# Performance work log

Hardware: AMD Instinct MI355X
Metric: run time of the kernel (lower is better)

## Reference

```python
import jax, jax.numpy as jnp
import numpy as np

B, N, D, E, H = 4, 1024, 1024, 8, 4096


def setup_inputs() -> dict:
    key = jax.random.key(0)
    ks = jax.random.split(key, 8)
    x = jax.random.normal(ks[0], (B, N, D), dtype=jnp.float32)
    # gumbel noise, matching F.gumbel_softmax's -log(-log(U))
    u = jax.random.uniform(ks[1], (B * N, E), dtype=jnp.float32, minval=1e-9, maxval=1.0)
    gumbel = -jnp.log(-jnp.log(u))
    router_w = jax.random.normal(ks[2], (D, E), dtype=jnp.float32) * 0.02
    router_b = jnp.zeros((E,), dtype=jnp.float32)
    w1 = jax.random.normal(ks[3], (E, D, H), dtype=jnp.float32) * 0.02
    b1 = jnp.zeros((E, H), dtype=jnp.float32)
    w2 = jax.random.normal(ks[4], (E, H, D), dtype=jnp.float32) * 0.02
    b2 = jnp.zeros((E, D), dtype=jnp.float32)
    return {"x": x, "gumbel": gumbel, "router_w": router_w, "router_b": router_b,
            "w1": w1, "b1": b1, "w2": w2, "b2": b2}


def reference(x, gumbel, router_w, router_b, w1, b1, w2, b2):
    b, n, d = x.shape
    e = router_w.shape[1]
    xf = x.reshape(-1, d)                      # (T, D), T = B*N tokens
    logits = xf @ router_w + router_b          # (T, E)

    # hard gumbel-softmax with straight-through estimator (tau = 1.0)
    y_soft = jax.nn.softmax(logits + gumbel, axis=-1)
    hard = jax.nn.one_hot(jnp.argmax(y_soft, axis=-1), e, dtype=y_soft.dtype)
    weights = hard - jax.lax.stop_gradient(y_soft) + y_soft   # (T, E)

    # load-balancing aux loss
    probs = jax.nn.softmax(logits, axis=-1)
    count = jnp.maximum(jnp.float32(xf.shape[0]), 1.0)
    importance = probs.sum(axis=0) / count
    aux_loss = jnp.mean((importance - 1.0 / e) ** 2)

    # dense all-expert FFN: every expert processes every token
    hidden = jax.nn.gelu(jnp.einsum('td,edh->eth', xf, w1) + b1[:, None, :],
                         approximate=False)                    # (E, T, H)
    expert_out = jnp.einsum('eth,ehd->etd', hidden, w2) + b2[:, None, :]  # (E, T, D)

    # weighted combine (einsum 'ej,ejd->jd' in the original)
    out = jnp.einsum('te,etd->td', weights, expert_out)        # (T, D)
    return out.reshape(b, n, d), aux_loss
```

## Files before the change

kernel.cpp:

```cpp
#include <hip/hip_runtime.h>
#include <math.h>

#define D_DIM 1024
#define MAX_TILES 40

typedef __attribute__((ext_vector_type(4))) float f32x4;
typedef __attribute__((ext_vector_type(8))) short s16x8;

__device__ __forceinline__ unsigned short f2bf(float f){
  union { float f; unsigned u; } v; v.f = f;
  unsigned r = v.u + 0x7FFFu + ((v.u >> 16) & 1u);
  return (unsigned short)(r >> 16);
}

__device__ __forceinline__ void gld_lds16(const unsigned short* g, unsigned short* l){
  __builtin_amdgcn_global_load_lds(
      (const __attribute__((address_space(1))) unsigned int*)g,
      (__attribute__((address_space(3))) unsigned int*)l, 16, 0, 0);
}

__global__ __launch_bounds__(256) void router_kernel(
    const float* __restrict__ x, const float* __restrict__ gumbel,
    const float* __restrict__ rw, const float* __restrict__ rb,
    int* __restrict__ expert_id, float* __restrict__ wtok,
    double* __restrict__ prob_sums, int* __restrict__ counts)
{
  int wave = threadIdx.x >> 6, lane = threadIdx.x & 63;
  int t = blockIdx.x * 4 + wave;
  const float* xr = x + (size_t)t * D_DIM;
  double acc[8];
  #pragma unroll
  for (int e = 0; e < 8; e++) acc[e] = 0.0;
  #pragma unroll
  for (int i = 0; i < 16; i++){
    int d = i * 64 + lane;
    double xv = (double)xr[d];
    const float4* rwp = (const float4*)(rw + (size_t)d * 8);
    float4 r0 = rwp[0], r1 = rwp[1];
    acc[0] += xv * (double)r0.x; acc[1] += xv * (double)r0.y;
    acc[2] += xv * (double)r0.z; acc[3] += xv * (double)r0.w;
    acc[4] += xv * (double)r1.x; acc[5] += xv * (double)r1.y;
    acc[6] += xv * (double)r1.z; acc[7] += xv * (double)r1.w;
  }
  #pragma unroll
  for (int e = 0; e < 8; e++){
    #pragma unroll
    for (int off = 32; off; off >>= 1) acc[e] += __shfl_xor(acc[e], off);
  }
  double logit[8], z[8];
  #pragma unroll
  for (int e = 0; e < 8; e++){
    logit[e] = acc[e] + (double)rb[e];
    z[e] = logit[e] + (double)gumbel[(size_t)t * 8 + e];
  }
  int amax = 0;
  #pragma unroll
  for (int e = 1; e < 8; e++) if (z[e] > z[amax]) amax = e;
  float zm = (float)z[amax];
  float se = 0.f;
  #pragma unroll
  for (int e = 0; e < 8; e++) se += expf((float)z[e] - zm);
  float y = 1.f / se;
  float w = (1.0f - y) + y;
  double lm = logit[0];
  #pragma unroll
  for (int e = 1; e < 8; e++) lm = fmax(lm, logit[e]);
  float p[8]; float ps = 0.f;
  #pragma unroll
  for (int e = 0; e < 8; e++){ p[e] = expf((float)(logit[e] - lm)); ps += p[e]; }
  float inv = 1.f / ps;

  __shared__ float sprob[4][8];
  if (lane == 0){
    expert_id[t] = amax; wtok[t] = w;
    atomicAdd(&counts[amax], 1);
    #pragma unroll
    for (int e = 0; e < 8; e++) sprob[wave][e] = p[e] * inv;
  }
  __syncthreads();
  if (threadIdx.x < 8){
    double s = (double)sprob[0][threadIdx.x] + (double)sprob[1][threadIdx.x]
             + (double)sprob[2][threadIdx.x] + (double)sprob[3][threadIdx.x];
    atomicAdd(&prob_sums[threadIdx.x], s);
  }
}

__global__ void finalize_kernel(const double* __restrict__ prob_sums, const int* __restrict__ counts,
                                int* __restrict__ offsets, int* __restrict__ cursor,
                                int* __restrict__ tile_e, int* __restrict__ tile_start,
                                int* __restrict__ tile_rows, int* __restrict__ n_mtiles,
                                float* __restrict__ aux_out)
{
  if (threadIdx.x == 0){
    int off = 0, m = 0;
    for (int e = 0; e < 8; e++){
      offsets[e] = off; cursor[e] = off;
      int c = counts[e];
      for (int by = 0; by * 128 < c; by++){
        tile_e[m] = e;
        tile_start[m] = off + by * 128;
        int r = c - by * 128;
        tile_rows[m] = r < 128 ? r : 128;
        m++;
      }
      off += c;
    }
    n_mtiles[0] = m;
    double aux = 0.0;
    for (int e = 0; e < 8; e++){
      double d = prob_sums[e] / 4096.0 - 0.125;
      aux += d * d;
    }
    aux_out[0] = (float)(aux / 8.0);
  }
}

__global__ __launch_bounds__(256) void scatter_kernel(
    const float* __restrict__ x, const int* __restrict__ expert_id, const float* __restrict__ wtok,
    int* __restrict__ cursor, int* __restrict__ token_of, float* __restrict__ gw,
    unsigned short* __restrict__ Xg)
{
  int t = blockIdx.x;
  __shared__ int spos;
  if (threadIdx.x == 0){
    int e = expert_id[t];
    int p = atomicAdd(&cursor[e], 1);
    spos = p;
    token_of[p] = t; gw[p] = wtok[t];
  }
  __syncthreads();
  int pos = spos;
  float4 v = ((const float4*)(x + (size_t)t * D_DIM))[threadIdx.x];
  ushort4 o; o.x = f2bf(v.x); o.y = f2bf(v.y); o.z = f2bf(v.z); o.w = f2bf(v.w);
  ((ushort4*)(Xg + (size_t)pos * D_DIM))[threadIdx.x] = o;
}

__global__ __launch_bounds__(256) void transpose_w(
    const float* __restrict__ W, unsigned short* __restrict__ WT, int K, int N)
{
  int e = blockIdx.z;
  int k0 = blockIdx.x * 64;
  int n0 = blockIdx.y * 64;
  __shared__ float tile[64][65];
  const float* src = W + (size_t)e * K * N;
  int tid = threadIdx.x;
  int r = tid >> 4;
  int c4 = (tid & 15) * 4;
  #pragma unroll
  for (int j = 0; j < 4; j++){
    int k = r + j * 16;
    float4 v = *(const float4*)(src + (size_t)(k0 + k) * N + n0 + c4);
    tile[k][c4] = v.x; tile[k][c4 + 1] = v.y; tile[k][c4 + 2] = v.z; tile[k][c4 + 3] = v.w;
  }
  __syncthreads();
  unsigned short* dst = WT + (size_t)e * N * K;
  int n = tid >> 2;
  #pragma unroll
  for (int h = 0; h < 2; h++){
    int s = (tid & 3) + h * 4;
    unsigned short buf[8];
    #pragma unroll
    for (int j = 0; j < 8; j++) buf[j] = f2bf(tile[s * 8 + j][n]);
    *(s16x8*)(dst + (size_t)(n0 + n) * K + k0 + s * 8) = *(s16x8*)buf;
  }
}

template<int K, int N, int BN, int PASS2>
__global__ __launch_bounds__(256, 2) void ffn_gemm(
    const unsigned short* __restrict__ A,
    const unsigned short* __restrict__ BT,
    const float* __restrict__ bias,
    const int* __restrict__ tile_e, const int* __restrict__ tile_start,
    const int* __restrict__ tile_rows, const int* __restrict__ n_mtiles,
    const int* __restrict__ token_of, const float* __restrict__ gw,
    unsigned short* __restrict__ Hout,
    float* __restrict__ Fout)
{
  int mt = blockIdx.y;
  if (mt >= n_mtiles[0]) return;
  int e = tile_e[mt], tstart = tile_start[mt], trows = tile_rows[mt];
  int bx = blockIdx.x;
  int tid = threadIdx.x, lane = tid & 63;
  int wv = __builtin_amdgcn_readfirstlane(tid >> 6);
  int wm = wv & 1, wn = wv >> 1;
  constexpr int NI  = BN / 32;
  constexpr int NBW = BN / 32;
  constexpr int NK  = K / 64;

  __shared__ unsigned short sA[2][128 * 64];
  __shared__ unsigned short sB[2][BN * 64];

  int r8  = lane >> 3;
  int swz = ((lane & 7) ^ r8) * 8;

  const unsigned short* ap[4]; int al[4];
  #pragma unroll
  for (int j = 0; j < 4; j++){
    int c = wv * 4 + j;
    int row = c * 8 + r8;
    int rr = row < trows ? row : 0;
    ap[j] = A + (size_t)(tstart + rr) * K + swz;
    al[j] = c * 512;
  }
  const unsigned short* bp[NBW]; int bl[NBW];
  #pragma unroll
  for (int j = 0; j < NBW; j++){
    int c = wv * NBW + j;
    int n = bx * BN + c * 8 + r8;
    bp[j] = BT + ((size_t)e * N + n) * K + swz;
    bl[j] = c * 512;
  }

  f32x4 accv[4][NI];
  #pragma unroll
  for (int mi = 0; mi < 4; mi++)
    #pragma unroll
    for (int ni = 0; ni < NI; ni++) accv[mi][ni] = (f32x4){0.f, 0.f, 0.f, 0.f};

  #pragma unroll
  for (int j = 0; j < 4; j++){ gld_lds16(ap[j], &sA[0][al[j]]); ap[j] += 64; }
  #pragma unroll
  for (int j = 0; j < NBW; j++){ gld_lds16(bp[j], &sB[0][bl[j]]); bp[j] += 64; }
  __syncthreads();

  int col = lane & 15, quad = lane >> 4, rx = col & 7;
  for (int kt = 0; kt < NK; ++kt){
    int cur = kt & 1;
    if (kt + 1 < NK){
      #pragma unroll
      for (int j = 0; j < 4; j++){ gld_lds16(ap[j], &sA[cur ^ 1][al[j]]); ap[j] += 64; }
      #pragma unroll
      for (int j = 0; j < NBW; j++){ gld_lds16(bp[j], &sB[cur ^ 1][bl[j]]); bp[j] += 64; }
    }
    #pragma unroll
    for (int kh = 0; kh < 2; kh++){
      int ps = ((kh * 4 + quad) ^ rx) * 8;
      s16x8 af[4], bfr[NI];
      #pragma unroll
      for (int mi = 0; mi < 4; mi++)
        af[mi] = *(const s16x8*)&sA[cur][(wm * 64 + mi * 16 + col) * 64 + ps];
      #pragma unroll
      for (int ni = 0; ni < NI; ni++)
        bfr[ni] = *(const s16x8*)&sB[cur][(wn * (BN / 2) + ni * 16 + col) * 64 + ps];
      #pragma unroll
      for (int mi = 0; mi < 4; mi++)
        #pragma unroll
        for (int ni = 0; ni < NI; ni++)
          accv[mi][ni] = __builtin_amdgcn_mfma_f32_16x16x32_bf16(af[mi], bfr[ni], accv[mi][ni], 0, 0, 0);
    }
    __syncthreads();
  }

  float bv[NI];
  #pragma unroll
  for (int ni = 0; ni < NI; ni++)
    bv[ni] = bias[(size_t)e * N + bx * BN + wn * (BN / 2) + ni * 16 + col];

  if (PASS2 == 0){
    #pragma unroll
    for (int mi = 0; mi < 4; mi++){
      int rbase = wm * 64 + mi * 16 + quad * 4;
      #pragma unroll
      for (int r = 0; r < 4; r++){
        int row = rbase + r;
        if (row < trows){
          size_t orow = (size_t)(tstart + row) * N + bx * BN + wn * (BN / 2) + col;
          #pragma unroll
          for (int ni = 0; ni < NI; ni++){
            float v = accv[mi][ni][r] + bv[ni];
            float g = 0.5f * v * (1.0f + erff(v * 0.70710678118654752f));
            Hout[orow + ni * 16] = f2bf(g);
          }
        }
      }
    }
  } else {
    #pragma unroll
    for (int mi = 0; mi < 4; mi++){
      int rbase = wm * 64 + mi * 16 + quad * 4;
      #pragma unroll
      for (int r = 0; r < 4; r++){
        int row = rbase + r;
        if (row < trows){
          int pos = tstart + row;
          int tok = token_of[pos];
          float wgt = gw[pos];
          size_t orow = (size_t)tok * N + bx * BN + wn * (BN / 2) + col;
          #pragma unroll
          for (int ni = 0; ni < NI; ni++)
            Fout[orow + ni * 16] = (accv[mi][ni][r] + bv[ni]) * wgt;
        }
      }
    }
  }
}

extern "C" void kernel_launch(void* const* d_in, const int* in_sizes, int n_in,
                              void* d_out, int out_size, void* d_ws, size_t ws_size,
                              hipStream_t stream)
{
  const float* x      = (const float*)d_in[0];
  const float* gumbel = (const float*)d_in[1];
  const float* rw     = (const float*)d_in[2];
  const float* rb     = (const float*)d_in[3];
  const float* w1     = (const float*)d_in[4];
  const float* b1     = (const float*)d_in[5];
  const float* w2     = (const float*)d_in[6];
  const float* b2     = (const float*)d_in[7];
  float* out = (float*)d_out;

  char* ws = (char*)d_ws;
  double* prob_sums = (double*)(ws + 0);
  int* counts     = (int*)(ws + 64);
  int* offsets    = (int*)(ws + 96);
  int* cursor     = (int*)(ws + 128);
  int* n_mtiles   = (int*)(ws + 160);
  int* tile_e     = (int*)(ws + 192);
  int* tile_start = (int*)(ws + 384);
  int* tile_rows  = (int*)(ws + 576);
  int* expert_id  = (int*)(ws + 1024);
  float* wtok     = (float*)(ws + 1024 + 16384);
  int* token_of   = (int*)(ws + 1024 + 2 * 16384);
  float* gw       = (float*)(ws + 1024 + 3 * 16384);
  unsigned short* Xg     = (unsigned short*)(ws + 66560);
  unsigned short* hidden = (unsigned short*)(ws + 66560 + 8388608);
  unsigned short* wT     = (unsigned short*)(ws + 66560 + 8388608 + 33554432);

  hipMemsetAsync(ws, 0, 256, stream);

  router_kernel<<<1024, 256, 0, stream>>>(x, gumbel, rw, rb, expert_id, wtok, prob_sums, counts);
  finalize_kernel<<<1, 64, 0, stream>>>(prob_sums, counts, offsets, cursor,
                                        tile_e, tile_start, tile_rows, n_mtiles, out + 4194304);
  scatter_kernel<<<4096, 256, 0, stream>>>(x, expert_id, wtok, cursor, token_of, gw, Xg);

  transpose_w<<<dim3(16, 64, 8), 256, 0, stream>>>(w1, wT, 1024, 4096);
  ffn_gemm<1024, 4096, 128, 0><<<dim3(32, MAX_TILES), 256, 0, stream>>>(
      Xg, wT, b1, tile_e, tile_start, tile_rows, n_mtiles, nullptr, nullptr, hidden, nullptr);

  transpose_w<<<dim3(64, 16, 8), 256, 0, stream>>>(w2, wT, 4096, 1024);
  ffn_gemm<4096, 1024, 64, 1><<<dim3(16, MAX_TILES), 256, 0, stream>>>(
      hidden, wT, b2, tile_e, tile_start, tile_rows, n_mtiles, token_of, gw, nullptr, out);
}
```

Baseline: 562.5 us.

## Restructure FFN GEMM main loop with explicit vmcnt waits and two-stage prefetch

The GEMM loop now issues loads for two K-tiles up front. Each iteration waits with s_waitcnt vmcnt on only the older batch, reads the whole tile's LDS fragments into registers, then does a barrier so the next-next tile can be loaded into the same buffer while MFMAs run at raised priority. This targets the full __syncthreads stall and exposes more of the global-to-LDS latency to overlap with compute. The weight-transpose kernel's store indexing is also remapped so consecutive threads write adjacent 16-byte chunks of a row. The cost is higher register pressure from holding both k-halves of fragments, and correctness now depends on hand-counted vmcnt values matching LOADS.

After: 544.8 us. 3.1% less time.

```diff
diff --git a/kernel.cpp b/kernel.cpp
--- a/kernel.cpp
+++ b/kernel.cpp
@@ -17,6 +17,14 @@
   __builtin_amdgcn_global_load_lds(
       (const __attribute__((address_space(1))) unsigned int*)g,
       (__attribute__((address_space(3))) unsigned int*)l, 16, 0, 0);
+}
+
+template<int N>
+__device__ __forceinline__ void wait_vmcnt(){
+  if constexpr (N == 8)      asm volatile("s_waitcnt vmcnt(8)" ::: "memory");
+  else if constexpr (N == 6) asm volatile("s_waitcnt vmcnt(6)" ::: "memory");
+  else                       asm volatile("s_waitcnt vmcnt(0)" ::: "memory");
+  __builtin_amdgcn_sched_barrier(0);
 }
 
 __global__ __launch_bounds__(256) void router_kernel(
@@ -154,10 +162,11 @@
   }
   __syncthreads();
   unsigned short* dst = WT + (size_t)e * N * K;
-  int n = tid >> 2;
-  #pragma unroll
-  for (int h = 0; h < 2; h++){
-    int s = (tid & 3) + h * 4;
+  #pragma unroll
+  for (int it = 0; it < 2; it++){
+    int idx = it * 256 + tid;
+    int n = idx >> 3;
+    int s = idx & 7;
     unsigned short buf[8];
     #pragma unroll
     for (int j = 0; j < 8; j++) buf[j] = f2bf(tile[s * 8 + j][n]);
@@ -183,9 +192,10 @@
   int tid = threadIdx.x, lane = tid & 63;
   int wv = __builtin_amdgcn_readfirstlane(tid >> 6);
   int wm = wv & 1, wn = wv >> 1;
-  constexpr int NI  = BN / 32;
-  constexpr int NBW = BN / 32;
-  constexpr int NK  = K / 64;
+  constexpr int NI    = BN / 32;
+  constexpr int NBW   = BN / 32;
+  constexpr int NK    = K / 64;
+  constexpr int LOADS = 4 + NBW;
 
   __shared__ unsigned short sA[2][128 * 64];
   __shared__ unsigned short sB[2][BN * 64];
@@ -218,37 +228,47 @@
     for (int ni = 0; ni < NI; ni++) accv[mi][ni] = (f32x4){0.f, 0.f, 0.f, 0.f};
 
   #pragma unroll
-  for (int j = 0; j < 4; j++){ gld_lds16(ap[j], &sA[0][al[j]]); ap[j] += 64; }
-  #pragma unroll
-  for (int j = 0; j < NBW; j++){ gld_lds16(bp[j], &sB[0][bl[j]]); bp[j] += 64; }
-  __syncthreads();
+  for (int b = 0; b < 2; b++){
+    #pragma unroll
+    for (int j = 0; j < 4; j++){ gld_lds16(ap[j], &sA[b][al[j]]); ap[j] += 64; }
+    #pragma unroll
+    for (int j = 0; j < NBW; j++){ gld_lds16(bp[j], &sB[b][bl[j]]); bp[j] += 64; }
+  }
 
   int col = lane & 15, quad = lane >> 4, rx = col & 7;
   for (int kt = 0; kt < NK; ++kt){
     int cur = kt & 1;
-    if (kt + 1 < NK){
-      #pragma unroll
-      for (int j = 0; j < 4; j++){ gld_lds16(ap[j], &sA[cur ^ 1][al[j]]); ap[j] += 64; }
-      #pragma unroll
-      for (int j = 0; j < NBW; j++){ gld_lds16(bp[j], &sB[cur ^ 1][bl[j]]); bp[j] += 64; }
-    }
+    if (kt + 1 < NK) wait_vmcnt<LOADS>(); else wait_vmcnt<0>();
+    __builtin_amdgcn_s_barrier();
+    s16x8 af[2][4], bfr[2][NI];
     #pragma unroll
     for (int kh = 0; kh < 2; kh++){
       int ps = ((kh * 4 + quad) ^ rx) * 8;
-      s16x8 af[4], bfr[NI];
       #pragma unroll
       for (int mi = 0; mi < 4; mi++)
-        af[mi] = *(const s16x8*)&sA[cur][(wm * 64 + mi * 16 + col) * 64 + ps];
+        af[kh][mi] = *(const s16x8*)&sA[cur][(wm * 64 + mi * 16 + col) * 64 + ps];
       #pragma unroll
       for (int ni = 0; ni < NI; ni++)
-        bfr[ni] = *(const s16x8*)&sB[cur][(wn * (BN / 2) + ni * 16 + col) * 64 + ps];
+        bfr[kh][ni] = *(const s16x8*)&sB[cur][(wn * (BN / 2) + ni * 16 + col) * 64 + ps];
+    }
+    asm volatile("s_waitcnt lgkmcnt(0)" ::: "memory");
+    __builtin_amdgcn_sched_barrier(0);
+    __builtin_amdgcn_s_barrier();
+    if (kt + 2 < NK){
+      #pragma unroll
+      for (int j = 0; j < 4; j++){ gld_lds16(ap[j], &sA[cur][al[j]]); ap[j] += 64; }
+      #pragma unroll
+      for (int j = 0; j < NBW; j++){ gld_lds16(bp[j], &sB[cur][bl[j]]); bp[j] += 64; }
+    }
+    __builtin_amdgcn_s_setprio(1);
+    #pragma unroll
+    for (int kh = 0; kh < 2; kh++)
       #pragma unroll
       for (int mi = 0; mi < 4; mi++)
         #pragma unroll
         for (int ni = 0; ni < NI; ni++)
-          accv[mi][ni] = __builtin_amdgcn_mfma_f32_16x16x32_bf16(af[mi], bfr[ni], accv[mi][ni], 0, 0, 0);
-    }
-    __syncthreads();
+          accv[mi][ni] = __builtin_amdgcn_mfma_f32_16x16x32_bf16(af[kh][mi], bfr[kh][ni], accv[mi][ni], 0, 0, 0);
+    __builtin_amdgcn_s_setprio(0);
   }
 
   float bv[NI];
```

## Fuse weight transpose and bf16 conversion into GEMM B-tile loading

Applied to the files above, without the earlier changes.

Removes the two separate transpose_w kernels that converted fp32 expert weights into transposed bf16 copies. The GEMM now reads fp32 weights straight from global memory into registers, converts them to bf16 and writes them transposed into swizzled LDS. It also restructures the main loop into a hand-scheduled software pipeline with explicit waitcnt, sched_barrier and setprio around the MFMA blocks. The aim is to avoid the separate transpose launches and their round trip through global memory, at the cost of more register pressure and each m-tile re-converting the weights it uses.

New measurement: 560.8 us. No clear change (-0.3%).

```diff
diff --git a/kernel.cpp b/kernel.cpp
--- a/kernel.cpp
+++ b/kernel.cpp
@@ -135,40 +135,10 @@
   ((ushort4*)(Xg + (size_t)pos * D_DIM))[threadIdx.x] = o;
 }
 
-__global__ __launch_bounds__(256) void transpose_w(
-    const float* __restrict__ W, unsigned short* __restrict__ WT, int K, int N)
-{
-  int e = blockIdx.z;
-  int k0 = blockIdx.x * 64;
-  int n0 = blockIdx.y * 64;
-  __shared__ float tile[64][65];
-  const float* src = W + (size_t)e * K * N;
-  int tid = threadIdx.x;
-  int r = tid >> 4;
-  int c4 = (tid & 15) * 4;
-  #pragma unroll
-  for (int j = 0; j < 4; j++){
-    int k = r + j * 16;
-    float4 v = *(const float4*)(src + (size_t)(k0 + k) * N + n0 + c4);
-    tile[k][c4] = v.x; tile[k][c4 + 1] = v.y; tile[k][c4 + 2] = v.z; tile[k][c4 + 3] = v.w;
-  }
-  __syncthreads();
-  unsigned short* dst = WT + (size_t)e * N * K;
-  int n = tid >> 2;
-  #pragma unroll
-  for (int h = 0; h < 2; h++){
-    int s = (tid & 3) + h * 4;
-    unsigned short buf[8];
-    #pragma unroll
-    for (int j = 0; j < 8; j++) buf[j] = f2bf(tile[s * 8 + j][n]);
-    *(s16x8*)(dst + (size_t)(n0 + n) * K + k0 + s * 8) = *(s16x8*)buf;
-  }
-}
-
 template<int K, int N, int BN, int PASS2>
 __global__ __launch_bounds__(256, 2) void ffn_gemm(
     const unsigned short* __restrict__ A,
-    const unsigned short* __restrict__ BT,
+    const float* __restrict__ W,
     const float* __restrict__ bias,
     const int* __restrict__ tile_e, const int* __restrict__ tile_start,
     const int* __restrict__ tile_rows, const int* __restrict__ n_mtiles,
@@ -184,31 +154,49 @@
   int wv = __builtin_amdgcn_readfirstlane(tid >> 6);
   int wm = wv & 1, wn = wv >> 1;
   constexpr int NI  = BN / 32;
-  constexpr int NBW = BN / 32;
+  constexpr int CPT = BN / 32;
   constexpr int NK  = K / 64;
 
   __shared__ unsigned short sA[2][128 * 64];
   __shared__ unsigned short sB[2][BN * 64];
 
   int r8  = lane >> 3;
-  int swz = ((lane & 7) ^ r8) * 8;
-
+  int swzA = ((lane & 7) ^ r8) * 8;
   const unsigned short* ap[4]; int al[4];
   #pragma unroll
   for (int j = 0; j < 4; j++){
     int c = wv * 4 + j;
     int row = c * 8 + r8;
     int rr = row < trows ? row : 0;
-    ap[j] = A + (size_t)(tstart + rr) * K + swz;
+    ap[j] = A + (size_t)(tstart + rr) * K + swzA;
     al[j] = c * 512;
   }
-  const unsigned short* bp[NBW]; int bl[NBW];
-  #pragma unroll
-  for (int j = 0; j < NBW; j++){
-    int c = wv * NBW + j;
-    int n = bx * BN + c * 8 + r8;
-    bp[j] = BT + ((size_t)e * N + n) * K + swz;
-    bl[j] = c * 512;
+
+  int bg = tid & 31;
+  int bs = tid >> 5;
+  const float* bsrc = W + (size_t)e * K * N + (size_t)(bs * 8) * N + (size_t)bx * BN + bg * CPT;
+  int bwoff[CPT];
+  #pragma unroll
+  for (int c = 0; c < CPT; c++){
+    int n_ = bg * CPT + c;
+    int slot_ = bs ^ ((n_ & 7) ^ ((n_ >> 3) & 7));
+    bwoff[c] = n_ * 64 + slot_ * 8;
+  }
+  float rB0[8][CPT], rB1[8][CPT];
+
+  int col = lane & 15, quad = lane >> 4;
+  int rowA[4], rowB[NI], psB0[NI], psB1[NI];
+  int psA0 = (quad ^ (col & 7)) * 8;
+  int psA1 = ((4 + quad) ^ (col & 7)) * 8;
+  #pragma unroll
+  for (int mi = 0; mi < 4; mi++) rowA[mi] = (wm * 64 + mi * 16 + col) * 64;
+  #pragma unroll
+  for (int ni = 0; ni < NI; ni++){
+    int n_ = wn * (BN / 2) + ni * 16 + col;
+    rowB[ni] = n_ * 64;
+    int sw = (n_ & 7) ^ ((n_ >> 3) & 7);
+    psB0[ni] = (quad ^ sw) * 8;
+    psB1[ni] = ((4 + quad) ^ sw) * 8;
   }
 
   f32x4 accv[4][NI];
@@ -217,39 +205,85 @@
     #pragma unroll
     for (int ni = 0; ni < NI; ni++) accv[mi][ni] = (f32x4){0.f, 0.f, 0.f, 0.f};
 
-  #pragma unroll
-  for (int j = 0; j < 4; j++){ gld_lds16(ap[j], &sA[0][al[j]]); ap[j] += 64; }
-  #pragma unroll
-  for (int j = 0; j < NBW; j++){ gld_lds16(bp[j], &sB[0][bl[j]]); bp[j] += 64; }
-  __syncthreads();
-
-  int col = lane & 15, quad = lane >> 4, rx = col & 7;
-  for (int kt = 0; kt < NK; ++kt){
-    int cur = kt & 1;
-    if (kt + 1 < NK){
-      #pragma unroll
-      for (int j = 0; j < 4; j++){ gld_lds16(ap[j], &sA[cur ^ 1][al[j]]); ap[j] += 64; }
-      #pragma unroll
-      for (int j = 0; j < NBW; j++){ gld_lds16(bp[j], &sB[cur ^ 1][bl[j]]); bp[j] += 64; }
-    }
-    #pragma unroll
-    for (int kh = 0; kh < 2; kh++){
-      int ps = ((kh * 4 + quad) ^ rx) * 8;
-      s16x8 af[4], bfr[NI];
-      #pragma unroll
-      for (int mi = 0; mi < 4; mi++)
-        af[mi] = *(const s16x8*)&sA[cur][(wm * 64 + mi * 16 + col) * 64 + ps];
-      #pragma unroll
-      for (int ni = 0; ni < NI; ni++)
-        bfr[ni] = *(const s16x8*)&sB[cur][(wn * (BN / 2) + ni * 16 + col) * 64 + ps];
-      #pragma unroll
-      for (int mi = 0; mi < 4; mi++)
-        #pragma unroll
-        for (int ni = 0; ni < NI; ni++)
-          accv[mi][ni] = __builtin_amdgcn_mfma_f32_16x16x32_bf16(af[mi], bfr[ni], accv[mi][ni], 0, 0, 0);
-    }
-    __syncthreads();
-  }
+#define A_ISSUE(BUF) { \
+  _Pragma("unroll") for (int j = 0; j < 4; j++){ gld_lds16(ap[j], &sA[BUF][al[j]]); ap[j] += 64; } \
+  __builtin_amdgcn_sched_barrier(0); }
+
+#define B_ISSUE(RB, KT) { \
+  const float* p_ = bsrc + (size_t)(KT) * 64 * N; \
+  _Pragma("unroll") for (int j = 0; j < 8; j++){ \
+    if constexpr (CPT == 4) *(f32x4*)&RB[j][0] = *(const f32x4*)(p_ + (size_t)j * N); \
+    else                    *(float2*)&RB[j][0] = *(const float2*)(p_ + (size_t)j * N); \
+  } \
+  __builtin_amdgcn_sched_barrier(0); }
+
+#define B_WRITE(RB, BUF) { \
+  _Pragma("unroll") for (int c = 0; c < CPT; c++){ \
+    unsigned short tw_[8]; \
+    _Pragma("unroll") for (int j = 0; j < 8; j++) tw_[j] = f2bf(RB[j][c]); \
+    *(s16x8*)&sB[BUF][bwoff[c]] = *(s16x8*)tw_; \
+  } }
+
+  B_ISSUE(rB0, 0);
+  A_ISSUE(0);
+  B_ISSUE(rB1, 1);
+  asm volatile("s_waitcnt vmcnt(12)" ::: "memory");
+  __builtin_amdgcn_sched_barrier(0);
+  B_WRITE(rB0, 0);
+  A_ISSUE(1);
+  asm volatile("s_waitcnt lgkmcnt(0)" ::: "memory");
+  __builtin_amdgcn_sched_barrier(0);
+
+#define FFN_STEP(ISSUE_RB, CONS_RB, KT) { \
+  const int cur_ = (KT) & 1; \
+  if ((KT) + 1 < NK) { asm volatile("s_waitcnt vmcnt(12)" ::: "memory"); } \
+  else               { asm volatile("s_waitcnt vmcnt(0)"  ::: "memory"); } \
+  __builtin_amdgcn_sched_barrier(0); \
+  __builtin_amdgcn_s_barrier(); \
+  if ((KT) + 2 < NK) { B_ISSUE(ISSUE_RB, (KT) + 2); } \
+  s16x8 af0[4], bf0[NI], af1[4], bf1[NI]; \
+  _Pragma("unroll") for (int mi = 0; mi < 4; mi++) \
+    af0[mi] = *(const s16x8*)&sA[cur_][rowA[mi] + psA0]; \
+  _Pragma("unroll") for (int ni = 0; ni < NI; ni++) \
+    bf0[ni] = *(const s16x8*)&sB[cur_][rowB[ni] + psB0[ni]]; \
+  asm volatile("s_waitcnt lgkmcnt(0)" ::: "memory"); \
+  __builtin_amdgcn_sched_barrier(0); \
+  __builtin_amdgcn_s_setprio(1); \
+  _Pragma("unroll") for (int mi = 0; mi < 4; mi++) \
+    _Pragma("unroll") for (int ni = 0; ni < NI; ni++) \
+      accv[mi][ni] = __builtin_amdgcn_mfma_f32_16x16x32_bf16(af0[mi], bf0[ni], accv[mi][ni], 0, 0, 0); \
+  __builtin_amdgcn_s_setprio(0); \
+  _Pragma("unroll") for (int mi = 0; mi < 4; mi++) \
+    af1[mi] = *(const s16x8*)&sA[cur_][rowA[mi] + psA1]; \
+  _Pragma("unroll") for (int ni = 0; ni < NI; ni++) \
+    bf1[ni] = *(const s16x8*)&sB[cur_][rowB[ni] + psB1[ni]]; \
+  if ((KT) + 1 < NK) { \
+    if ((KT) + 2 < NK) { asm volatile("s_waitcnt vmcnt(12)" ::: "memory"); } \
+    else               { asm volatile("s_waitcnt vmcnt(4)"  ::: "memory"); } \
+    __builtin_amdgcn_sched_barrier(0); \
+    B_WRITE(CONS_RB, cur_ ^ 1); \
+  } \
+  asm volatile("s_waitcnt lgkmcnt(0)" ::: "memory"); \
+  __builtin_amdgcn_sched_barrier(0); \
+  __builtin_amdgcn_s_barrier(); \
+  if ((KT) + 2 < NK) { A_ISSUE(cur_); } \
+  __builtin_amdgcn_s_setprio(1); \
+  _Pragma("unroll") for (int mi = 0; mi < 4; mi++) \
+    _Pragma("unroll") for (int ni = 0; ni < NI; ni++) \
+      accv[mi][ni] = __builtin_amdgcn_mfma_f32_16x16x32_bf16(af1[mi], bf1[ni], accv[mi][ni], 0, 0, 0); \
+  __builtin_amdgcn_s_setprio(0); \
+}
+
+  #pragma unroll 1
+  for (int kt = 0; kt < NK; kt += 2){
+    FFN_STEP(rB0, rB1, kt);
+    FFN_STEP(rB1, rB0, kt + 1);
+  }
+
+#undef FFN_STEP
+#undef B_WRITE
+#undef B_ISSUE
+#undef A_ISSUE
 
   float bv[NI];
   #pragma unroll
@@ -324,7 +358,6 @@
   float* gw       = (float*)(ws + 1024 + 3 * 16384);
   unsigned short* Xg     = (unsigned short*)(ws + 66560);
   unsigned short* hidden = (unsigned short*)(ws + 66560 + 8388608);
-  unsigned short* wT     = (unsigned short*)(ws + 66560 + 8388608 + 33554432);
 
   hipMemsetAsync(ws, 0, 256, stream);
 
@@ -333,11 +366,9 @@
                                         tile_e, tile_start, tile_rows, n_mtiles, out + 4194304);
   scatter_kernel<<<4096, 256, 0, stream>>>(x, expert_id, wtok, cursor, token_of, gw, Xg);
 
-  transpose_w<<<dim3(16, 64, 8), 256, 0, stream>>>(w1, wT, 1024, 4096);
   ffn_gemm<1024, 4096, 128, 0><<<dim3(32, MAX_TILES), 256, 0, stream>>>(
-      Xg, wT, b1, tile_e, tile_start, tile_rows, n_mtiles, nullptr, nullptr, hidden, nullptr);
-
-  transpose_w<<<dim3(64, 16, 8), 256, 0, stream>>>(w2, wT, 4096, 1024);
+      Xg, w1, b1, tile_e, tile_start, tile_rows, n_mtiles, nullptr, nullptr, hidden, nullptr);
+
   ffn_gemm<4096, 1024, 64, 1><<<dim3(16, MAX_TILES), 256, 0, stream>>>(
-      hidden, wT, b2, tile_e, tile_start, tile_rows, n_mtiles, token_of, gw, nullptr, out);
-}
+      hidden, w2, b2, tile_e, tile_start, tile_rows, n_mtiles, token_of, gw, nullptr, out);
+}
```
